# Optimization experiments

Measured on AMD Instinct MI355X. Metric: run time of the kernel, lower is better.

The kernel has to match this reference:

```python
import jax, jax.numpy as jnp
import numpy as np

DIM = 1024
HEADS = 8
NUM_EXPERTS = 65536
NUM_KEYS = 256  # sqrt(NUM_EXPERTS)
DIM_KEY = 512
TOPK = 16  # product_key_topk == num_experts_per_head


def setup_inputs() -> dict:
    key = jax.random.key(0)
    ks = jax.random.split(key, 6)
    B, N = 2, 512
    x = jax.random.normal(ks[0], (B, N, DIM), dtype=jnp.float32)
    gamma = jnp.ones((DIM,), dtype=jnp.float32)
    wq = jax.random.normal(ks[1], (2 * HEADS * DIM_KEY, DIM), dtype=jnp.float32) * 0.02
    keys = jax.random.normal(ks[2], (HEADS, NUM_KEYS, 2, DIM_KEY), dtype=jnp.float32) * 0.02
    table_down = jax.random.normal(ks[3], (NUM_EXPERTS, DIM), dtype=jnp.float32) * 0.02
    table_up = jax.random.normal(ks[4], (NUM_EXPERTS, DIM), dtype=jnp.float32) * 0.02
    return {"x": x, "gamma": gamma, "wq": wq, "keys": keys,
            "table_down": table_down, "table_up": table_up}


def _rmsnorm(v, g):
    # torch F.normalize(x, dim=-1) * gamma * sqrt(dim)
    scale = jnp.sqrt(jnp.asarray(v.shape[-1], v.dtype))
    n = jnp.maximum(jnp.linalg.norm(v, axis=-1, keepdims=True), 1e-12)
    return v / n * g * scale


def reference(x, gamma, wq, keys, table_down, table_up):
    B, N, D = x.shape
    xn = _rmsnorm(x, gamma)          # pre_rmsnorm on x
    gate = xn                        # x_in_gate is None -> gate = norm(x)
    # queries: b n (p h d) -> p b n h d
    q = gate @ wq.T                  # [B,N,2*H*DK]
    q = q.reshape(B, N, 2, HEADS, DIM_KEY).transpose(2, 0, 1, 3, 4)  # [2,B,N,H,DK]
    # sim: p b n h d, h k p d -> p b n h k
    sim = jnp.einsum('pbnhd,hkpd->pbnhk', q, keys)
    sx, ix = jax.lax.top_k(sim[0], TOPK)  # [B,N,H,TOPK]
    sy, iy = jax.lax.top_k(sim[1], TOPK)
    # outer sums over the two product-key axes -> [B,N,H,TOPK*TOPK]
    all_scores = (sx[..., :, None] + sy[..., None, :]).reshape(B, N, HEADS, TOPK * TOPK)
    all_indices = (ix[..., :, None] * NUM_KEYS + iy[..., None, :]).reshape(B, N, HEADS, TOPK * TOPK)
    scores, pk = jax.lax.top_k(all_scores, TOPK)           # [B,N,H,K]
    indices = jnp.take_along_axis(all_indices, pk, axis=-1)  # expert ids [B,N,H,K]
    wd = table_down[indices]  # [B,N,H,K,D]
    wu = table_up[indices]    # [B,N,H,K,D]
    h = jnp.einsum('bnd,bnhkd->bnhk', xn, wd)
    h = jax.nn.gelu(h, approximate=False) * jax.nn.softmax(scores, axis=-1)
    out = jnp.einsum('bnhk,bnhkd->bnd', h, wu)
    return out
```

## Files before the change

kernel.cpp:

```cpp
#include <hip/hip_runtime.h>
#include <math.h>


#define DIMV 1024

__global__ __launch_bounds__(256) void peer_rmsnorm(const float* __restrict__ x,
                                                    const float* __restrict__ gamma,
                                                    float* __restrict__ xnf)
{
    int t = blockIdx.x;
    int tid = threadIdx.x;
    const float4* xr = (const float4*)(x + (size_t)t * DIMV);
    float4 v = xr[tid];
    double ss = (double)v.x*v.x + (double)v.y*v.y + (double)v.z*v.z + (double)v.w*v.w;
    #pragma unroll
    for (int off = 32; off > 0; off >>= 1) ss += __shfl_xor(ss, off);
    __shared__ double red[4];
    if ((tid & 63) == 0) red[tid >> 6] = ss;
    __syncthreads();
    double tot = red[0] + red[1] + red[2] + red[3];
    float n32 = (float)fmax(sqrt(tot), 1e-12);
    const float4* g4 = (const float4*)gamma;
    float4 gv = g4[tid];
    float4 o;
    o.x = __fmul_rn(__fmul_rn(__fdiv_rn(v.x, n32), gv.x), 32.0f);
    o.y = __fmul_rn(__fmul_rn(__fdiv_rn(v.y, n32), gv.y), 32.0f);
    o.z = __fmul_rn(__fmul_rn(__fdiv_rn(v.z, n32), gv.z), 32.0f);
    o.w = __fmul_rn(__fmul_rn(__fdiv_rn(v.w, n32), gv.w), 32.0f);
    ((float4*)(xnf + (size_t)t * DIMV))[tid] = o;
}

__global__ __launch_bounds__(128) void peer_qgemm(const float* __restrict__ A,
                                                  const float* __restrict__ Bm,
                                                  float* __restrict__ C)
{
    __shared__ float As[2][16][128];
    __shared__ float Bs[2][16][64];
    int tid = threadIdx.x;
    int n0 = blockIdx.x * 64, m0 = blockIdx.y * 128;
    int tx = tid & 7, ty = tid >> 3;
    int rb = tid >> 1, lk8 = (tid & 1) * 8;
    float acc[8][8] = {};
    float4 av0 = *(const float4*)(A  + (long)(m0 + tid) * 1024 + 0);
    float4 av1 = *(const float4*)(A  + (long)(m0 + tid) * 1024 + 4);
    float4 av2 = *(const float4*)(A  + (long)(m0 + tid) * 1024 + 8);
    float4 av3 = *(const float4*)(A  + (long)(m0 + tid) * 1024 + 12);
    float4 bv0 = *(const float4*)(Bm + (long)(n0 + rb) * 1024 + lk8);
    float4 bv1 = *(const float4*)(Bm + (long)(n0 + rb) * 1024 + lk8 + 4);
    #pragma unroll
    for (int j = 0; j < 4; j++) {
        As[0][j][tid]      = ((const float*)&av0)[j];
        As[0][4 + j][tid]  = ((const float*)&av1)[j];
        As[0][8 + j][tid]  = ((const float*)&av2)[j];
        As[0][12 + j][tid] = ((const float*)&av3)[j];
        Bs[0][lk8 + j][rb]     = ((const float*)&bv0)[j];
        Bs[0][lk8 + 4 + j][rb] = ((const float*)&bv1)[j];
    }
    __syncthreads();
    int cur = 0;
    for (int k0 = 0; k0 < 1024; k0 += 16) {
        bool more = (k0 + 16) < 1024;
        if (more) {
            av0 = *(const float4*)(A  + (long)(m0 + tid) * 1024 + (k0 + 16));
            av1 = *(const float4*)(A  + (long)(m0 + tid) * 1024 + (k0 + 20));
            av2 = *(const float4*)(A  + (long)(m0 + tid) * 1024 + (k0 + 24));
            av3 = *(const float4*)(A  + (long)(m0 + tid) * 1024 + (k0 + 28));
            bv0 = *(const float4*)(Bm + (long)(n0 + rb) * 1024 + (k0 + 16 + lk8));
            bv1 = *(const float4*)(Bm + (long)(n0 + rb) * 1024 + (k0 + 20 + lk8));
        }
        #pragma unroll
        for (int kk = 0; kk < 16; kk++) {
            float4 a0 = *(const float4*)&As[cur][kk][ty * 8];
            float4 a1 = *(const float4*)&As[cur][kk][ty * 8 + 4];
            float4 b0 = *(const float4*)&Bs[cur][kk][tx * 8];
            float4 b1 = *(const float4*)&Bs[cur][kk][tx * 8 + 4];
            float ra8[8] = {a0.x,a0.y,a0.z,a0.w, a1.x,a1.y,a1.z,a1.w};
            float rb8[8] = {b0.x,b0.y,b0.z,b0.w, b1.x,b1.y,b1.z,b1.w};
            #pragma unroll
            for (int i = 0; i < 8; i++)
                #pragma unroll
                for (int j = 0; j < 8; j++)
                    acc[i][j] = __fmaf_rn(ra8[i], rb8[j], acc[i][j]);
        }
        if (more) {
            int nxt = cur ^ 1;
            #pragma unroll
            for (int j = 0; j < 4; j++) {
                As[nxt][j][tid]      = ((const float*)&av0)[j];
                As[nxt][4 + j][tid]  = ((const float*)&av1)[j];
                As[nxt][8 + j][tid]  = ((const float*)&av2)[j];
                As[nxt][12 + j][tid] = ((const float*)&av3)[j];
                Bs[nxt][lk8 + j][rb]     = ((const float*)&bv0)[j];
                Bs[nxt][lk8 + 4 + j][rb] = ((const float*)&bv1)[j];
            }
            __syncthreads();
            cur = nxt;
        }
    }
    #pragma unroll
    for (int i = 0; i < 8; i++) {
        float4 c0 = {acc[i][0], acc[i][1], acc[i][2], acc[i][3]};
        float4 c1 = {acc[i][4], acc[i][5], acc[i][6], acc[i][7]};
        long r = (long)(m0 + ty * 8 + i) * 8192 + (n0 + tx * 8);
        *(float4*)(C + r)     = c0;
        *(float4*)(C + r + 4) = c1;
    }
}

__global__ __launch_bounds__(256) void peer_sim(const float* __restrict__ qf,
                                                const float* __restrict__ keys,
                                                float* __restrict__ simf)
{
    int tb = blockIdx.x;
    int z  = blockIdx.y;
    int h = z & 7, p = z >> 3;
    int tid = threadIdx.x;
    __shared__ float4 qs[16][128];
    int t0 = tb * 16;
    long qbase = (long)h * 512 + (long)p * 4096;
    int row = tid >> 4, c0 = (tid & 15) * 8;
    const float4* qrow = (const float4*)(qf + (long)(t0 + row) * 8192 + qbase);
    #pragma unroll
    for (int u = 0; u < 8; u++) qs[row][c0 + u] = qrow[c0 + u];
    __syncthreads();
    int k = tid;
    const float4* krow = (const float4*)(keys + (long)h * 262144 + (long)k * 1024 + (long)p * 512);
    float pa[16][4] = {};
    for (int d4 = 0; d4 < 128; d4++) {
        float4 kv = krow[d4];
        #pragma unroll
        for (int tt = 0; tt < 16; tt++) {
            float4 qv = qs[tt][d4];
            pa[tt][0] = __fadd_rn(pa[tt][0], __fmul_rn(qv.x, kv.x));
            pa[tt][1] = __fadd_rn(pa[tt][1], __fmul_rn(qv.y, kv.y));
            pa[tt][2] = __fadd_rn(pa[tt][2], __fmul_rn(qv.z, kv.z));
            pa[tt][3] = __fadd_rn(pa[tt][3], __fmul_rn(qv.w, kv.w));
        }
    }
    #pragma unroll
    for (int tt = 0; tt < 16; tt++) {
        float s = __fadd_rn(__fadd_rn(pa[tt][0], pa[tt][2]),
                            __fadd_rn(pa[tt][1], pa[tt][3]));
        simf[(long)(t0 + tt) * 4096 + (long)p * 2048 + h * 256 + k] = s;
    }
}

__device__ inline void peer_select16(float v[4], int lane, float* outv, int* outi)
{
    for (int iter = 0; iter < 16; iter++) {
        float bv = -INFINITY; int bk = 1 << 30;
        #pragma unroll
        for (int i = 0; i < 4; i++) {
            int k = i * 64 + lane;
            if (v[i] > bv || (v[i] == bv && k < bk)) { bv = v[i]; bk = k; }
        }
        #pragma unroll
        for (int off = 32; off > 0; off >>= 1) {
            float ov = __shfl_xor(bv, off);
            int   ok = __shfl_xor(bk, off);
            if (ov > bv || (ov == bv && ok < bk)) { bv = ov; bk = ok; }
        }
        if (lane == 0) { outv[iter] = bv; outi[iter] = bk; }
        __syncthreads();
        if ((bk & 63) == lane) v[bk >> 6] = -INFINITY;
    }
}

__global__ __launch_bounds__(64) void peer_topk(const float* __restrict__ sim,
                                                float* __restrict__ wsel,
                                                int* __restrict__ esel)
{
    int b = blockIdx.x;
    int t = b >> 3, h = b & 7;
    int lane = threadIdx.x;
    const float* simx = sim + (size_t)t * 4096 + h * 256;
    const float* simy = simx + 2048;
    __shared__ float sxv[16]; __shared__ int sxi[16];
    __shared__ float syv[16]; __shared__ int syi[16];
    __shared__ float cv[16];  __shared__ int cf[16];
    float v[4];
    #pragma unroll
    for (int i = 0; i < 4; i++) v[i] = simx[i*64 + lane];
    peer_select16(v, lane, sxv, sxi);
    __syncthreads();
    #pragma unroll
    for (int i = 0; i < 4; i++) v[i] = simy[i*64 + lane];
    peer_select16(v, lane, syv, syi);
    __syncthreads();
    #pragma unroll
    for (int i = 0; i < 4; i++) {
        int f = i*64 + lane;
        v[i] = __fadd_rn(sxv[f >> 4], syv[f & 15]);
    }
    peer_select16(v, lane, cv, cf);
    __syncthreads();
    double m = (double)cv[0];
    double w = (lane < 16) ? exp((double)cv[lane] - m) : 0.0;
    double Z = w;
    #pragma unroll
    for (int off = 32; off > 0; off >>= 1) Z += __shfl_xor(Z, off);
    if (lane < 16) {
        int f = cf[lane];
        esel[b * 16 + lane] = sxi[f >> 4] * 256 + syi[f & 15];
        wsel[b * 16 + lane] = (float)(w / Z);
    }
}

__global__ __launch_bounds__(256) void peer_downup(const float* __restrict__ xn,
                                                   const float* __restrict__ table_down,
                                                   const float* __restrict__ table_up,
                                                   const int* __restrict__ esel,
                                                   const float* __restrict__ wsel,
                                                   float* __restrict__ out)
{
    int t = blockIdx.x;
    int tid = threadIdx.x;
    int wid = tid >> 6, lane = tid & 63;
    __shared__ float4 xs[256];
    __shared__ float  gs[128];
    __shared__ int    es[128];
    if (tid < 128) es[tid] = esel[t * 128 + tid];
    xs[tid] = ((const float4*)(xn + (size_t)t * DIMV))[tid];
    __syncthreads();
    int base = wid * 32;
    const float4* dr = (const float4*)(table_down + (size_t)es[base] * DIMV);
    float4 p0 = dr[lane], p1 = dr[64 + lane], p2 = dr[128 + lane], p3 = dr[192 + lane];
    float4 a0 = xs[lane], a1 = xs[64 + lane], a2 = xs[128 + lane], a3 = xs[192 + lane];
    for (int jj = 0; jj < 32; jj++) {
        float4 c0 = p0, c1 = p1, c2 = p2, c3 = p3;
        if (jj < 31) {
            const float4* nr = (const float4*)(table_down + (size_t)es[base + jj + 1] * DIMV);
            p0 = nr[lane]; p1 = nr[64 + lane]; p2 = nr[128 + lane]; p3 = nr[192 + lane];
        }
        double acc = 0.0;
        acc = fma((double)a0.x, (double)c0.x, acc);
        acc = fma((double)a0.y, (double)c0.y, acc);
        acc = fma((double)a0.z, (double)c0.z, acc);
        acc = fma((double)a0.w, (double)c0.w, acc);
        acc = fma((double)a1.x, (double)c1.x, acc);
        acc = fma((double)a1.y, (double)c1.y, acc);
        acc = fma((double)a1.z, (double)c1.z, acc);
        acc = fma((double)a1.w, (double)c1.w, acc);
        acc = fma((double)a2.x, (double)c2.x, acc);
        acc = fma((double)a2.y, (double)c2.y, acc);
        acc = fma((double)a2.z, (double)c2.z, acc);
        acc = fma((double)a2.w, (double)c2.w, acc);
        acc = fma((double)a3.x, (double)c3.x, acc);
        acc = fma((double)a3.y, (double)c3.y, acc);
        acc = fma((double)a3.z, (double)c3.z, acc);
        acc = fma((double)a3.w, (double)c3.w, acc);
        #pragma unroll
        for (int off = 32; off > 0; off >>= 1) acc += __shfl_xor(acc, off);
        if (lane == 0) {
            double hv = acc;
            double ge = 0.5 * hv * (1.0 + erf(hv * 0.70710678118654752));
            gs[base + jj] = (float)(ge * (double)wsel[t * 128 + base + jj]);
        }
    }
    __syncthreads();
    int dbase = tid * 4;
    double b0 = 0, b1 = 0, b2 = 0, b3 = 0;
    float4 u0 = *(const float4*)(table_up + (size_t)es[0] * DIMV + dbase);
    float4 u1 = *(const float4*)(table_up + (size_t)es[1] * DIMV + dbase);
    float4 u2 = *(const float4*)(table_up + (size_t)es[2] * DIMV + dbase);
    float4 u3 = *(const float4*)(table_up + (size_t)es[3] * DIMV + dbase);
    for (int j = 0; j < 128; j += 4) {
        float4 c0 = u0, c1 = u1, c2 = u2, c3 = u3;
        if (j + 4 < 128) {
            u0 = *(const float4*)(table_up + (size_t)es[j + 4] * DIMV + dbase);
            u1 = *(const float4*)(table_up + (size_t)es[j + 5] * DIMV + dbase);
            u2 = *(const float4*)(table_up + (size_t)es[j + 6] * DIMV + dbase);
            u3 = *(const float4*)(table_up + (size_t)es[j + 7] * DIMV + dbase);
        }
        double g0 = (double)gs[j],     g1 = (double)gs[j + 1];
        double g2 = (double)gs[j + 2], g3 = (double)gs[j + 3];
        b0 = fma(g0, (double)c0.x, b0); b1 = fma(g0, (double)c0.y, b1);
        b2 = fma(g0, (double)c0.z, b2); b3 = fma(g0, (double)c0.w, b3);
        b0 = fma(g1, (double)c1.x, b0); b1 = fma(g1, (double)c1.y, b1);
        b2 = fma(g1, (double)c1.z, b2); b3 = fma(g1, (double)c1.w, b3);
        b0 = fma(g2, (double)c2.x, b0); b1 = fma(g2, (double)c2.y, b1);
        b2 = fma(g2, (double)c2.z, b2); b3 = fma(g2, (double)c2.w, b3);
        b0 = fma(g3, (double)c3.x, b0); b1 = fma(g3, (double)c3.y, b1);
        b2 = fma(g3, (double)c3.z, b2); b3 = fma(g3, (double)c3.w, b3);
    }
    float4 o = {(float)b0, (float)b1, (float)b2, (float)b3};
    *(float4*)(out + (size_t)t * DIMV + dbase) = o;
}

extern "C" void kernel_launch(void* const* d_in, const int* in_sizes, int n_in,
                              void* d_out, int out_size, void* d_ws, size_t ws_size,
                              hipStream_t stream)
{
    const float* x          = (const float*)d_in[0];
    const float* gamma      = (const float*)d_in[1];
    const float* wq         = (const float*)d_in[2];
    const float* keys       = (const float*)d_in[3];
    const float* table_down = (const float*)d_in[4];
    const float* table_up   = (const float*)d_in[5];
    float* out = (float*)d_out;
    char* wsb  = (char*)d_ws;

    float* xnf  = (float*)(wsb);
    float* qf   = (float*)(wsb + (4ull<<20));
    float* simf = (float*)(wsb + (36ull<<20));
    float* wsel = (float*)(wsb + (52ull<<20));
    int*   esel = (int*)  (wsb + (52ull<<20) + (512ull<<10));
    if (ws_size < (54ull << 20)) return;

    peer_rmsnorm<<<1024, 256, 0, stream>>>(x, gamma, xnf);

    peer_qgemm<<<dim3(128, 8, 1), 128, 0, stream>>>(xnf, wq, qf);

    peer_sim<<<dim3(64, 16, 1), 256, 0, stream>>>(qf, keys, simf);

    peer_topk<<<8192, 64, 0, stream>>>(simf, wsel, esel);

    peer_downup<<<1024, 256, 0, stream>>>(xnf, table_down, table_up,
                                          esel, wsel, out);
}
```

Baseline: 570.0 us.

## Enlarge qgemm tiles to 128x128x32 and double downup block threads

The Q projection GEMM now uses 256 threads computing 128x128 output tiles with a K-step of 32. This raises arithmetic intensity and halves the number of blocks, and the B fragment reads are changed to strided float4 reads. The down/up expert kernel now runs 512 threads: each wave handles 16 experts instead of 32 for the down projection, and each thread accumulates 2 output columns instead of 4. Together these aim to increase latency hiding for the gather-bound phase, at the cost of more LDS per GEMM block and possibly lower occupancy.

```diff
diff --git a/kernel.cpp b/kernel.cpp
--- a/kernel.cpp
+++ b/kernel.cpp
@@ -30,50 +30,56 @@
     ((float4*)(xnf + (size_t)t * DIMV))[tid] = o;
 }
 
-__global__ __launch_bounds__(128) void peer_qgemm(const float* __restrict__ A,
+__global__ __launch_bounds__(256) void peer_qgemm(const float* __restrict__ A,
                                                   const float* __restrict__ Bm,
                                                   float* __restrict__ C)
 {
-    __shared__ float As[2][16][128];
-    __shared__ float Bs[2][16][64];
+    __shared__ float As[2][32][128];
+    __shared__ float Bs[2][32][128];
     int tid = threadIdx.x;
-    int n0 = blockIdx.x * 64, m0 = blockIdx.y * 128;
-    int tx = tid & 7, ty = tid >> 3;
-    int rb = tid >> 1, lk8 = (tid & 1) * 8;
+    int m0 = blockIdx.y * 128, n0 = blockIdx.x * 128;
+    int tx = tid & 15, ty = tid >> 4;
+    int lrow = tid >> 1, lk16 = (tid & 1) * 16;
     float acc[8][8] = {};
-    float4 av0 = *(const float4*)(A  + (long)(m0 + tid) * 1024 + 0);
-    float4 av1 = *(const float4*)(A  + (long)(m0 + tid) * 1024 + 4);
-    float4 av2 = *(const float4*)(A  + (long)(m0 + tid) * 1024 + 8);
-    float4 av3 = *(const float4*)(A  + (long)(m0 + tid) * 1024 + 12);
-    float4 bv0 = *(const float4*)(Bm + (long)(n0 + rb) * 1024 + lk8);
-    float4 bv1 = *(const float4*)(Bm + (long)(n0 + rb) * 1024 + lk8 + 4);
+    float4 av0 = *(const float4*)(A  + (long)(m0 + lrow) * 1024 + lk16);
+    float4 av1 = *(const float4*)(A  + (long)(m0 + lrow) * 1024 + lk16 + 4);
+    float4 av2 = *(const float4*)(A  + (long)(m0 + lrow) * 1024 + lk16 + 8);
+    float4 av3 = *(const float4*)(A  + (long)(m0 + lrow) * 1024 + lk16 + 12);
+    float4 bv0 = *(const float4*)(Bm + (long)(n0 + lrow) * 1024 + lk16);
+    float4 bv1 = *(const float4*)(Bm + (long)(n0 + lrow) * 1024 + lk16 + 4);
+    float4 bv2 = *(const float4*)(Bm + (long)(n0 + lrow) * 1024 + lk16 + 8);
+    float4 bv3 = *(const float4*)(Bm + (long)(n0 + lrow) * 1024 + lk16 + 12);
     #pragma unroll
     for (int j = 0; j < 4; j++) {
-        As[0][j][tid]      = ((const float*)&av0)[j];
-        As[0][4 + j][tid]  = ((const float*)&av1)[j];
-        As[0][8 + j][tid]  = ((const float*)&av2)[j];
-        As[0][12 + j][tid] = ((const float*)&av3)[j];
-        Bs[0][lk8 + j][rb]     = ((const float*)&bv0)[j];
-        Bs[0][lk8 + 4 + j][rb] = ((const float*)&bv1)[j];
+        As[0][lk16 + j][lrow]      = ((const float*)&av0)[j];
+        As[0][lk16 + 4 + j][lrow]  = ((const float*)&av1)[j];
+        As[0][lk16 + 8 + j][lrow]  = ((const float*)&av2)[j];
+        As[0][lk16 + 12 + j][lrow] = ((const float*)&av3)[j];
+        Bs[0][lk16 + j][lrow]      = ((const float*)&bv0)[j];
+        Bs[0][lk16 + 4 + j][lrow]  = ((const float*)&bv1)[j];
+        Bs[0][lk16 + 8 + j][lrow]  = ((const float*)&bv2)[j];
+        Bs[0][lk16 + 12 + j][lrow] = ((const float*)&bv3)[j];
     }
     __syncthreads();
     int cur = 0;
-    for (int k0 = 0; k0 < 1024; k0 += 16) {
-        bool more = (k0 + 16) < 1024;
+    for (int k0 = 0; k0 < 1024; k0 += 32) {
+        bool more = (k0 + 32) < 1024;
         if (more) {
-            av0 = *(const float4*)(A  + (long)(m0 + tid) * 1024 + (k0 + 16));
-            av1 = *(const float4*)(A  + (long)(m0 + tid) * 1024 + (k0 + 20));
-            av2 = *(const float4*)(A  + (long)(m0 + tid) * 1024 + (k0 + 24));
-            av3 = *(const float4*)(A  + (long)(m0 + tid) * 1024 + (k0 + 28));
-            bv0 = *(const float4*)(Bm + (long)(n0 + rb) * 1024 + (k0 + 16 + lk8));
-            bv1 = *(const float4*)(Bm + (long)(n0 + rb) * 1024 + (k0 + 20 + lk8));
-        }
-        #pragma unroll
-        for (int kk = 0; kk < 16; kk++) {
+            av0 = *(const float4*)(A  + (long)(m0 + lrow) * 1024 + (k0 + 32 + lk16));
+            av1 = *(const float4*)(A  + (long)(m0 + lrow) * 1024 + (k0 + 36 + lk16));
+            av2 = *(const float4*)(A  + (long)(m0 + lrow) * 1024 + (k0 + 40 + lk16));
+            av3 = *(const float4*)(A  + (long)(m0 + lrow) * 1024 + (k0 + 44 + lk16));
+            bv0 = *(const float4*)(Bm + (long)(n0 + lrow) * 1024 + (k0 + 32 + lk16));
+            bv1 = *(const float4*)(Bm + (long)(n0 + lrow) * 1024 + (k0 + 36 + lk16));
+            bv2 = *(const float4*)(Bm + (long)(n0 + lrow) * 1024 + (k0 + 40 + lk16));
+            bv3 = *(const float4*)(Bm + (long)(n0 + lrow) * 1024 + (k0 + 44 + lk16));
+        }
+        #pragma unroll
+        for (int kk = 0; kk < 32; kk++) {
             float4 a0 = *(const float4*)&As[cur][kk][ty * 8];
             float4 a1 = *(const float4*)&As[cur][kk][ty * 8 + 4];
-            float4 b0 = *(const float4*)&Bs[cur][kk][tx * 8];
-            float4 b1 = *(const float4*)&Bs[cur][kk][tx * 8 + 4];
+            float4 b0 = *(const float4*)&Bs[cur][kk][tx * 4];
+            float4 b1 = *(const float4*)&Bs[cur][kk][tx * 4 + 64];
             float ra8[8] = {a0.x,a0.y,a0.z,a0.w, a1.x,a1.y,a1.z,a1.w};
             float rb8[8] = {b0.x,b0.y,b0.z,b0.w, b1.x,b1.y,b1.z,b1.w};
             #pragma unroll
@@ -86,12 +92,14 @@
             int nxt = cur ^ 1;
             #pragma unroll
             for (int j = 0; j < 4; j++) {
-                As[nxt][j][tid]      = ((const float*)&av0)[j];
-                As[nxt][4 + j][tid]  = ((const float*)&av1)[j];
-                As[nxt][8 + j][tid]  = ((const float*)&av2)[j];
-                As[nxt][12 + j][tid] = ((const float*)&av3)[j];
-                Bs[nxt][lk8 + j][rb]     = ((const float*)&bv0)[j];
-                Bs[nxt][lk8 + 4 + j][rb] = ((const float*)&bv1)[j];
+                As[nxt][lk16 + j][lrow]      = ((const float*)&av0)[j];
+                As[nxt][lk16 + 4 + j][lrow]  = ((const float*)&av1)[j];
+                As[nxt][lk16 + 8 + j][lrow]  = ((const float*)&av2)[j];
+                As[nxt][lk16 + 12 + j][lrow] = ((const float*)&av3)[j];
+                Bs[nxt][lk16 + j][lrow]      = ((const float*)&bv0)[j];
+                Bs[nxt][lk16 + 4 + j][lrow]  = ((const float*)&bv1)[j];
+                Bs[nxt][lk16 + 8 + j][lrow]  = ((const float*)&bv2)[j];
+                Bs[nxt][lk16 + 12 + j][lrow] = ((const float*)&bv3)[j];
             }
             __syncthreads();
             cur = nxt;
@@ -101,9 +109,9 @@
     for (int i = 0; i < 8; i++) {
         float4 c0 = {acc[i][0], acc[i][1], acc[i][2], acc[i][3]};
         float4 c1 = {acc[i][4], acc[i][5], acc[i][6], acc[i][7]};
-        long r = (long)(m0 + ty * 8 + i) * 8192 + (n0 + tx * 8);
-        *(float4*)(C + r)     = c0;
-        *(float4*)(C + r + 4) = c1;
+        long r = (long)(m0 + ty * 8 + i) * 8192 + n0;
+        *(float4*)(C + r + tx * 4)      = c0;
+        *(float4*)(C + r + 64 + tx * 4) = c1;
     }
 }
 
@@ -206,7 +214,7 @@
     }
 }
 
-__global__ __launch_bounds__(256) void peer_downup(const float* __restrict__ xn,
+__global__ __launch_bounds__(512) void peer_downup(const float* __restrict__ xn,
                                                    const float* __restrict__ table_down,
                                                    const float* __restrict__ table_up,
                                                    const int* __restrict__ esel,
@@ -220,15 +228,15 @@
     __shared__ float  gs[128];
     __shared__ int    es[128];
     if (tid < 128) es[tid] = esel[t * 128 + tid];
-    xs[tid] = ((const float4*)(xn + (size_t)t * DIMV))[tid];
-    __syncthreads();
-    int base = wid * 32;
+    if (tid < 256) xs[tid] = ((const float4*)(xn + (size_t)t * DIMV))[tid];
+    __syncthreads();
+    int base = wid * 16;
     const float4* dr = (const float4*)(table_down + (size_t)es[base] * DIMV);
     float4 p0 = dr[lane], p1 = dr[64 + lane], p2 = dr[128 + lane], p3 = dr[192 + lane];
     float4 a0 = xs[lane], a1 = xs[64 + lane], a2 = xs[128 + lane], a3 = xs[192 + lane];
-    for (int jj = 0; jj < 32; jj++) {
+    for (int jj = 0; jj < 16; jj++) {
         float4 c0 = p0, c1 = p1, c2 = p2, c3 = p3;
-        if (jj < 31) {
+        if (jj < 15) {
             const float4* nr = (const float4*)(table_down + (size_t)es[base + jj + 1] * DIMV);
             p0 = nr[lane]; p1 = nr[64 + lane]; p2 = nr[128 + lane]; p3 = nr[192 + lane];
         }
@@ -258,33 +266,29 @@
         }
     }
     __syncthreads();
-    int dbase = tid * 4;
-    double b0 = 0, b1 = 0, b2 = 0, b3 = 0;
-    float4 u0 = *(const float4*)(table_up + (size_t)es[0] * DIMV + dbase);
-    float4 u1 = *(const float4*)(table_up + (size_t)es[1] * DIMV + dbase);
-    float4 u2 = *(const float4*)(table_up + (size_t)es[2] * DIMV + dbase);
-    float4 u3 = *(const float4*)(table_up + (size_t)es[3] * DIMV + dbase);
+    int dbase = tid * 2;
+    double b0 = 0, b1 = 0;
+    float2 u0 = *(const float2*)(table_up + (size_t)es[0] * DIMV + dbase);
+    float2 u1 = *(const float2*)(table_up + (size_t)es[1] * DIMV + dbase);
+    float2 u2 = *(const float2*)(table_up + (size_t)es[2] * DIMV + dbase);
+    float2 u3 = *(const float2*)(table_up + (size_t)es[3] * DIMV + dbase);
     for (int j = 0; j < 128; j += 4) {
-        float4 c0 = u0, c1 = u1, c2 = u2, c3 = u3;
+        float2 c0 = u0, c1 = u1, c2 = u2, c3 = u3;
         if (j + 4 < 128) {
-            u0 = *(const float4*)(table_up + (size_t)es[j + 4] * DIMV + dbase);
-            u1 = *(const float4*)(table_up + (size_t)es[j + 5] * DIMV + dbase);
-            u2 = *(const float4*)(table_up + (size_t)es[j + 6] * DIMV + dbase);
-            u3 = *(const float4*)(table_up + (size_t)es[j + 7] * DIMV + dbase);
+            u0 = *(const float2*)(table_up + (size_t)es[j + 4] * DIMV + dbase);
+            u1 = *(const float2*)(table_up + (size_t)es[j + 5] * DIMV + dbase);
+            u2 = *(const float2*)(table_up + (size_t)es[j + 6] * DIMV + dbase);
+            u3 = *(const float2*)(table_up + (size_t)es[j + 7] * DIMV + dbase);
         }
         double g0 = (double)gs[j],     g1 = (double)gs[j + 1];
         double g2 = (double)gs[j + 2], g3 = (double)gs[j + 3];
         b0 = fma(g0, (double)c0.x, b0); b1 = fma(g0, (double)c0.y, b1);
-        b2 = fma(g0, (double)c0.z, b2); b3 = fma(g0, (double)c0.w, b3);
         b0 = fma(g1, (double)c1.x, b0); b1 = fma(g1, (double)c1.y, b1);
-        b2 = fma(g1, (double)c1.z, b2); b3 = fma(g1, (double)c1.w, b3);
         b0 = fma(g2, (double)c2.x, b0); b1 = fma(g2, (double)c2.y, b1);
-        b2 = fma(g2, (double)c2.z, b2); b3 = fma(g2, (double)c2.w, b3);
         b0 = fma(g3, (double)c3.x, b0); b1 = fma(g3, (double)c3.y, b1);
-        b2 = fma(g3, (double)c3.z, b2); b3 = fma(g3, (double)c3.w, b3);
-    }
-    float4 o = {(float)b0, (float)b1, (float)b2, (float)b3};
-    *(float4*)(out + (size_t)t * DIMV + dbase) = o;
+    }
+    float2 o = {(float)b0, (float)b1};
+    *(float2*)(out + (size_t)t * DIMV + dbase) = o;
 }
 
 extern "C" void kernel_launch(void* const* d_in, const int* in_sizes, int n_in,
@@ -309,12 +313,12 @@
 
     peer_rmsnorm<<<1024, 256, 0, stream>>>(x, gamma, xnf);
 
-    peer_qgemm<<<dim3(128, 8, 1), 128, 0, stream>>>(xnf, wq, qf);
+    peer_qgemm<<<dim3(64, 8, 1), 256, 0, stream>>>(xnf, wq, qf);
 
     peer_sim<<<dim3(64, 16, 1), 256, 0, stream>>>(qf, keys, simf);
 
     peer_topk<<<8192, 64, 0, stream>>>(simf, wsel, esel);
 
-    peer_downup<<<1024, 256, 0, stream>>>(xnf, table_down, table_up,
+    peer_downup<<<1024, 512, 0, stream>>>(xnf, table_down, table_up,
                                           esel, wsel, out);
 }
```

Measured after the change: 590.3 us. 3.6% more time.
